# Kernel tuning notes

Hardware: AMD Instinct MI355X
Metric: run time of the kernel (lower is better)

Reference implementation:

```python
import jax, jax.numpy as jnp
import numpy as np

D_IN = 1024
D_OUT = 1024
NUM_HEADS = 16
HEAD_DIM = D_OUT // NUM_HEADS


def setup_inputs() -> dict:
    key = jax.random.key(0)
    ks = jax.random.split(key, 6)
    s = 0.02
    x = jax.random.normal(ks[0], (2, 2048, D_IN), dtype=jnp.float32)
    Wq = jax.random.normal(ks[1], (D_IN, D_OUT), dtype=jnp.float32) * s
    Wk = jax.random.normal(ks[2], (D_IN, D_OUT), dtype=jnp.float32) * s
    Wv = jax.random.normal(ks[3], (D_IN, D_OUT), dtype=jnp.float32) * s
    Wo = jax.random.normal(ks[4], (D_OUT, D_OUT), dtype=jnp.float32) * s
    bo = jnp.zeros((D_OUT,), dtype=jnp.float32)
    return {"x": x, "Wq": Wq, "Wk": Wk, "Wv": Wv, "Wo": Wo, "bo": bo}


def reference(x, Wq, Wk, Wv, Wo, bo):
    b, n, _ = x.shape
    # project and split heads: [b, h, n, d]
    def heads(W):
        return (x @ W).reshape(b, n, NUM_HEADS, HEAD_DIM).transpose(0, 2, 1, 3)
    q, k, v = heads(Wq), heads(Wk), heads(Wv)
    scores = jnp.einsum("bhqd,bhkd->bhqk", q, k)  # [b,h,n,n]
    causal = jnp.tril(jnp.ones((n, n), dtype=bool))  # True = keep
    scores = jnp.where(causal, scores, -jnp.inf)
    attn = jax.nn.softmax(scores / np.sqrt(HEAD_DIM).astype(np.float32), axis=-1)
    ctx = jnp.einsum("bhqk,bhkd->bhqd", attn, v)
    ctx = ctx.transpose(0, 2, 1, 3).reshape(b, n, D_OUT)
    return ctx @ Wo + bo
```

## Files before the change

### kernel.cpp

```cpp
#include <hip/hip_runtime.h>
#include <stdint.h>

typedef unsigned short u16;
typedef __attribute__((ext_vector_type(8))) __bf16 bf16x8;
typedef __attribute__((ext_vector_type(4))) float f32x4;
typedef __attribute__((ext_vector_type(16))) float f32x16;

#define D_IN 1024
#define NH 16
#define DH 64
#define BATCH 2
#define SEQ 2048

#define QSCL 0.1803368801111244f

#define GLD_LDS16(gp, lp)                                                              \
  __builtin_amdgcn_global_load_lds((__attribute__((address_space(1))) const void*)(gp), \
                                   (__attribute__((address_space(3))) void*)(lp), 16, 0, 0)

__device__ __forceinline__ u16 f2b(float f) {
  union { float ff; uint32_t u; } v; v.ff = f;
  return (u16)((v.u + 0x7fffu + ((v.u >> 16) & 1u)) >> 16);
}

__device__ __forceinline__ float swap32f(float v) { return __shfl_xor(v, 32, 64); }

__device__ __forceinline__ uint32_t cvtpk(float a, float b) {
  uint32_t r;
  asm("v_cvt_pk_bf16_f32 %0, %1, %2" : "=v"(r) : "v"(a), "v"(b));
  return r;
}
__device__ __forceinline__ float fexp2(float x) {
  float r;
  asm("v_exp_f32 %0, %1" : "=v"(r) : "v"(x));
  return r;
}

__global__ __launch_bounds__(256)
void prep_kernel(const float* __restrict__ x, u16* __restrict__ xb,
                 const float* __restrict__ W0, const float* __restrict__ W1,
                 const float* __restrict__ W2, const float* __restrict__ W3,
                 u16* __restrict__ T0, u16* __restrict__ T1,
                 u16* __restrict__ T2, u16* __restrict__ T3) {
  __shared__ float tile[32][33];
  if (blockIdx.x < 4096) {
    const int i = (blockIdx.x * 256 + threadIdx.x) * 4;
    const float4 v = *(const float4*)(x + i);
    uint2 pack;
    pack.x = (uint32_t)f2b(v.x) | ((uint32_t)f2b(v.y) << 16);
    pack.y = (uint32_t)f2b(v.z) | ((uint32_t)f2b(v.w) << 16);
    *(uint2*)(xb + i) = pack;
  } else {
    const int bid2 = blockIdx.x - 4096;
    const float* W; u16* T;
    switch (bid2 >> 10) {
      case 0: W = W0; T = T0; break;
      case 1: W = W1; T = T1; break;
      case 2: W = W2; T = T2; break;
      default: W = W3; T = T3; break;
    }
    const int rem = bid2 & 1023;
    const int n0 = (rem >> 5) * 32, k0 = (rem & 31) * 32;
    const int tx = threadIdx.x & 31, ty = threadIdx.x >> 5;
    #pragma unroll
    for (int i = 0; i < 32; i += 8)
      tile[ty + i][tx] = W[(size_t)(k0 + ty + i) * D_IN + n0 + tx];
    __syncthreads();
    #pragma unroll
    for (int i = 0; i < 32; i += 8)
      T[(size_t)(n0 + ty + i) * D_IN + k0 + tx] = f2b(tile[tx][ty + i]);
  }
}

__device__ __forceinline__ void qkv_compute(
    const u16* __restrict__ AsB, const u16* __restrict__ Bq,
    const u16* __restrict__ Bk, const u16* __restrict__ Bv,
    int wm, int wn, int g, int lm,
    f32x4 accq[4][2], f32x4 acck[4][2], f32x4 accv[4][2]) {
  #pragma unroll
  for (int kk = 0; kk < 2; ++kk) {
    const int slot = ((kk * 4 + g) ^ (lm & 7)) << 3;
    bf16x8 af[4];
    #pragma unroll
    for (int i = 0; i < 4; ++i)
      af[i] = *(const bf16x8*)(AsB + (wm * 64 + i * 16 + lm) * 64 + slot);
    bf16x8 bq[2], bk[2], bv[2];
    #pragma unroll
    for (int n = 0; n < 2; ++n) {
      const int ro = (wn * 32 + n * 16 + lm) * 64 + slot;
      bq[n] = *(const bf16x8*)(Bq + ro);
      bk[n] = *(const bf16x8*)(Bk + ro);
      bv[n] = *(const bf16x8*)(Bv + ro);
    }
    #pragma unroll
    for (int i = 0; i < 4; ++i)
      #pragma unroll
      for (int n = 0; n < 2; ++n) {
        accq[i][n] = __builtin_amdgcn_mfma_f32_16x16x32_bf16(af[i], bq[n], accq[i][n], 0, 0, 0);
        acck[i][n] = __builtin_amdgcn_mfma_f32_16x16x32_bf16(af[i], bk[n], acck[i][n], 0, 0, 0);
        accv[i][n] = __builtin_amdgcn_mfma_f32_16x16x32_bf16(af[i], bv[n], accv[i][n], 0, 0, 0);
      }
  }
}

__global__ __launch_bounds__(512)
void gemm_qkv_kernel(const u16* __restrict__ Xb,
                     const u16* __restrict__ WqT, const u16* __restrict__ WkT,
                     const u16* __restrict__ WvT,
                     u16* __restrict__ Qo, u16* __restrict__ Ko, u16* __restrict__ Vt) {
  __shared__ u16 As[2][128 * 64];
  __shared__ u16 Bs[2][3][128 * 64];

  const int tid = threadIdx.x;
  const int lane = tid & 63;
  const int w = tid >> 6;
  const int wm = w >> 2, wn = w & 3;
  const int bm = blockIdx.x * 128;
  const int bn = blockIdx.y * 128;
  const int g = lane >> 4, lm = lane & 15;

  const int r_in = lane >> 3;
  const int s_w = lane & 7;
  const int swz_col = (s_w ^ r_in) << 3;

  const int c0 = w * 2;
  const u16* a_src0 = Xb + (size_t)(bm + c0 * 8 + r_in) * D_IN + swz_col;
  const u16* a_src1 = a_src0 + 8 * D_IN;
  const u16* q_src0 = WqT + (size_t)(bn + c0 * 8 + r_in) * D_IN + swz_col;
  const u16* q_src1 = q_src0 + 8 * D_IN;
  const u16* k_src0 = WkT + (size_t)(bn + c0 * 8 + r_in) * D_IN + swz_col;
  const u16* k_src1 = k_src0 + 8 * D_IN;
  const u16* v_src0 = WvT + (size_t)(bn + c0 * 8 + r_in) * D_IN + swz_col;
  const u16* v_src1 = v_src0 + 8 * D_IN;

#define QKV_STAGE(BUF, K0)                                 \
  do {                                                     \
    GLD_LDS16(a_src0 + (K0), &As[BUF][c0 * 512]);          \
    GLD_LDS16(a_src1 + (K0), &As[BUF][c0 * 512 + 512]);    \
    GLD_LDS16(q_src0 + (K0), &Bs[BUF][0][c0 * 512]);       \
    GLD_LDS16(q_src1 + (K0), &Bs[BUF][0][c0 * 512 + 512]); \
    GLD_LDS16(k_src0 + (K0), &Bs[BUF][1][c0 * 512]);       \
    GLD_LDS16(k_src1 + (K0), &Bs[BUF][1][c0 * 512 + 512]); \
    GLD_LDS16(v_src0 + (K0), &Bs[BUF][2][c0 * 512]);       \
    GLD_LDS16(v_src1 + (K0), &Bs[BUF][2][c0 * 512 + 512]); \
  } while (0)

  f32x4 accq[4][2], acck[4][2], accv[4][2];
  #pragma unroll
  for (int i = 0; i < 4; ++i)
    #pragma unroll
    for (int n = 0; n < 2; ++n) {
      accq[i][n] = {0.f, 0.f, 0.f, 0.f};
      acck[i][n] = {0.f, 0.f, 0.f, 0.f};
      accv[i][n] = {0.f, 0.f, 0.f, 0.f};
    }

  QKV_STAGE(0, 0);
  QKV_STAGE(1, 64);
  #pragma unroll 1
  for (int tt = 0; tt < 7; ++tt) {
    asm volatile("s_waitcnt vmcnt(8)" ::: "memory");
    __builtin_amdgcn_s_barrier();
    qkv_compute(As[0], Bs[0][0], Bs[0][1], Bs[0][2], wm, wn, g, lm, accq, acck, accv);
    __builtin_amdgcn_s_barrier();
    QKV_STAGE(0, (2 * tt + 2) * 64);
    asm volatile("s_waitcnt vmcnt(8)" ::: "memory");
    __builtin_amdgcn_s_barrier();
    qkv_compute(As[1], Bs[1][0], Bs[1][1], Bs[1][2], wm, wn, g, lm, accq, acck, accv);
    __builtin_amdgcn_s_barrier();
    QKV_STAGE(1, (2 * tt + 3) * 64);
  }
  asm volatile("s_waitcnt vmcnt(8)" ::: "memory");
  __builtin_amdgcn_s_barrier();
  qkv_compute(As[0], Bs[0][0], Bs[0][1], Bs[0][2], wm, wn, g, lm, accq, acck, accv);
  asm volatile("s_waitcnt vmcnt(0)" ::: "memory");
  __builtin_amdgcn_s_barrier();
  qkv_compute(As[1], Bs[1][0], Bs[1][1], Bs[1][2], wm, wn, g, lm, accq, acck, accv);
#undef QKV_STAGE

  #pragma unroll
  for (int i = 0; i < 4; ++i) {
    #pragma unroll
    for (int n = 0; n < 2; ++n) {
      #pragma unroll
      for (int r = 0; r < 4; ++r) {
        const int m = bm + wm * 64 + i * 16 + g * 4 + r;
        const int c = bn + wn * 32 + n * 16 + lm;
        const int b = m >> 11, nn = m & (SEQ - 1);
        const int h = c >> 6, d = c & (DH - 1);
        const int bh = b * NH + h;
        const int t = nn >> 5;
        {
          const u16 val = f2b(accq[i][n][r] * QSCL);
          const int st = d >> 4;
          const int lane2 = ((d >> 3) & 1) * 32 + (nn & 31);
          const int j = d & 7;
          Qo[((size_t)(bh * 64 + t) * 4 + st) * 512 + lane2 * 8 + j] = val;
        }
        {
          const u16 val = f2b(acck[i][n][r]);
          const int st = d >> 4;
          const int lane2 = ((d >> 3) & 1) * 32 + (nn & 31);
          const int j = d & 7;
          Ko[((size_t)(bh * 64 + t) * 4 + st) * 512 + lane2 * 8 + j] = val;
        }
        {
          const u16 val = f2b(accv[i][n][r]);
          const int n5 = nn & 31;
          const int f = (n5 >> 4) * 2 + (d >> 5);
          const int lane2 = ((n5 >> 2) & 1) * 32 + (d & 31);
          const int j = ((n5 >> 3) & 1) * 4 + (n5 & 3);
          Vt[((size_t)(bh * 64 + t) * 4 + f) * 512 + lane2 * 8 + j] = val;
        }
      }
    }
  }
}

__global__ __launch_bounds__(256)
void attn4_kernel(const u16* __restrict__ Qb, const u16* __restrict__ Kb,
                  const u16* __restrict__ Vt, u16* __restrict__ Ctx) {
  __shared__ float mbuf[4][32][64];
  __shared__ float lbuf[4][32];

  const int tid = threadIdx.x;
  const int lane = tid & 63;
  const int kw = tid >> 6;
  const int ql = lane & 31;
  const int hi = lane >> 5;
  const int bid = blockIdx.x;
  const int c = bid & 7;
  const int r = bid >> 3;
  const int jj = r & 31;
  const int bh = c + 8 * (r >> 5);
  const int b = bh >> 4, h = bh & 15;

  const u16* Qf = Qb + (size_t)bh * 64 * 2048;
  const u16* Kf = Kb + (size_t)bh * 64 * 2048;
  const u16* Vf = Vt + (size_t)bh * 64 * 2048;
  const int lofs = lane * 8;

  #pragma unroll 1
  for (int pass = 0; pass < 2; ++pass) {
    const int qt = pass ? (63 - jj) : jj;
    const int qb0 = qt * 32;

    bf16x8 qf[4];
    {
      const u16* qp = Qf + (size_t)qt * 2048 + lofs;
      #pragma unroll
      for (int st = 0; st < 4; ++st) qf[st] = *(const bf16x8*)(qp + st * 512);
    }

    f32x16 ctx0 = {0,0,0,0,0,0,0,0,0,0,0,0,0,0,0,0};
    f32x16 ctx1 = {0,0,0,0,0,0,0,0,0,0,0,0,0,0,0,0};
    float lacc[4] = {0.f, 0.f, 0.f, 0.f};

    bf16x8 kf[4], vf[4];
    if (kw <= qt) {
      {
        const u16* kp = Kf + (size_t)kw * 2048 + lofs;
        const u16* vp = Vf + (size_t)kw * 2048 + lofs;
        #pragma unroll
        for (int st = 0; st < 4; ++st) kf[st] = *(const bf16x8*)(kp + st * 512);
        #pragma unroll
        for (int f = 0; f < 4; ++f) vf[f] = *(const bf16x8*)(vp + f * 512);
      }
      #pragma unroll 2
      for (int t = kw; t <= qt; t += 4) {
        f32x16 s = {0,0,0,0,0,0,0,0,0,0,0,0,0,0,0,0};
        __builtin_amdgcn_s_setprio(1);
        #pragma unroll
        for (int st = 0; st < 4; ++st)
          s = __builtin_amdgcn_mfma_f32_32x32x16_bf16(kf[st], qf[st], s, 0, 0, 0);
        __builtin_amdgcn_s_setprio(0);

        const int tn = (t + 4 <= qt) ? (t + 4) : qt;
        {
          const u16* kp = Kf + (size_t)tn * 2048 + lofs;
          #pragma unroll
          for (int st = 0; st < 4; ++st) kf[st] = *(const bf16x8*)(kp + st * 512);
        }

        float p[16];
        if (t == qt) {
          #pragma unroll
          for (int cr = 0; cr < 16; ++cr) {
            const int kl = ((cr & 3) + 8 * (cr >> 2)) + 4 * hi;
            p[cr] = (kl > ql) ? 0.f : fexp2(s[cr]);
          }
        } else {
          #pragma unroll
          for (int cr = 0; cr < 16; ++cr) p[cr] = fexp2(s[cr]);
        }
        #pragma unroll
        for (int cr = 0; cr < 16; ++cr) lacc[cr & 3] += p[cr];

        __builtin_amdgcn_s_setprio(1);
        #pragma unroll
        for (int ks = 0; ks < 2; ++ks) {
          uint4 pw;
          pw.x = cvtpk(p[ks * 8 + 0], p[ks * 8 + 1]);
          pw.y = cvtpk(p[ks * 8 + 2], p[ks * 8 + 3]);
          pw.z = cvtpk(p[ks * 8 + 4], p[ks * 8 + 5]);
          pw.w = cvtpk(p[ks * 8 + 6], p[ks * 8 + 7]);
          union { uint4 u; bf16x8 v; } pa; pa.u = pw;
          ctx0 = __builtin_amdgcn_mfma_f32_32x32x16_bf16(vf[ks * 2 + 0], pa.v, ctx0, 0, 0, 0);
          ctx1 = __builtin_amdgcn_mfma_f32_32x32x16_bf16(vf[ks * 2 + 1], pa.v, ctx1, 0, 0, 0);
        }
        __builtin_amdgcn_s_setprio(0);

        {
          const u16* vp = Vf + (size_t)tn * 2048 + lofs;
          #pragma unroll
          for (int f = 0; f < 4; ++f) vf[f] = *(const bf16x8*)(vp + f * 512);
        }
      }
    }

    const float lloc = (lacc[0] + lacc[1]) + (lacc[2] + lacc[3]);
    const float lwv = lloc + swap32f(lloc);

    #pragma unroll
    for (int grp = 0; grp < 4; ++grp) {
      const int ch = grp * 2 + hi;
      f32x4 t0 = {ctx0[grp * 4 + 0], ctx0[grp * 4 + 1], ctx0[grp * 4 + 2], ctx0[grp * 4 + 3]};
      f32x4 t1 = {ctx1[grp * 4 + 0], ctx1[grp * 4 + 1], ctx1[grp * 4 + 2], ctx1[grp * 4 + 3]};
      *(f32x4*)&mbuf[kw][ql][(ch ^ ql) * 4 & 63]       = t0;
      *(f32x4*)&mbuf[kw][ql][((ch + 8) ^ ql) * 4 & 63] = t1;
    }
    if (lane < 32) lbuf[kw][ql] = lwv;
    __syncthreads();

    {
      const int ch0 = kw * 4 + hi * 2;
      f32x4 a0 = {0.f, 0.f, 0.f, 0.f}, a1 = {0.f, 0.f, 0.f, 0.f};
      #pragma unroll
      for (int p2 = 0; p2 < 4; ++p2) {
        a0 += *(const f32x4*)&mbuf[p2][ql][(ch0 ^ ql) * 4 & 63];
        a1 += *(const f32x4*)&mbuf[p2][ql][((ch0 + 1) ^ ql) * 4 & 63];
      }
      const float lt = (lbuf[0][ql] + lbuf[1][ql]) + (lbuf[2][ql] + lbuf[3][ql]);
      const float inv = __builtin_amdgcn_rcpf(lt);
      uint4 pw;
      pw.x = cvtpk(a0[0] * inv, a0[1] * inv);
      pw.y = cvtpk(a0[2] * inv, a0[3] * inv);
      pw.z = cvtpk(a1[0] * inv, a1[1] * inv);
      pw.w = cvtpk(a1[2] * inv, a1[3] * inv);
      *(uint4*)(Ctx + (size_t)(b * SEQ + qb0 + ql) * 1024 + h * 64 + kw * 16 + hi * 8) = pw;
    }
    __syncthreads();
  }
}

__device__ __forceinline__ void out_compute(
    const u16* __restrict__ AsB, const u16* __restrict__ BsB,
    int wr, int wc, int g, int lm, f32x4 acc[4][4]) {
  #pragma unroll
  for (int kk = 0; kk < 2; ++kk) {
    const int slot = ((kk * 4 + g) ^ (lm & 7)) << 3;
    bf16x8 af[4], bf[4];
    #pragma unroll
    for (int i = 0; i < 4; ++i)
      af[i] = *(const bf16x8*)(AsB + (wr * 64 + i * 16 + lm) * 64 + slot);
    #pragma unroll
    for (int n = 0; n < 4; ++n)
      bf[n] = *(const bf16x8*)(BsB + (wc * 64 + n * 16 + lm) * 64 + slot);
    #pragma unroll
    for (int i = 0; i < 4; ++i)
      #pragma unroll
      for (int n = 0; n < 4; ++n)
        acc[i][n] = __builtin_amdgcn_mfma_f32_16x16x32_bf16(af[i], bf[n], acc[i][n], 0, 0, 0);
  }
}

__global__ __launch_bounds__(256)
void gemm_out_kernel(const u16* __restrict__ Ctx, const u16* __restrict__ WoT,
                     const float* __restrict__ bo, float* __restrict__ out) {
  __shared__ u16 As[2][128 * 64];
  __shared__ u16 Bs[2][128 * 64];
  const int tid = threadIdx.x;
  const int lane = tid & 63;
  const int w = tid >> 6;
  const int bm = blockIdx.x * 128;
  const int bn = blockIdx.y * 128;
  const int wr = w >> 1, wc = w & 1;
  const int g = lane >> 4, lm = lane & 15;

  const int r_in = lane >> 3;
  const int s_w = lane & 7;
  const int swz_col = (s_w ^ r_in) << 3;

  const int c0 = w * 4;
  const u16* a_src = Ctx + (size_t)(bm + c0 * 8 + r_in) * D_IN + swz_col;
  const u16* b_src = WoT + (size_t)(bn + c0 * 8 + r_in) * D_IN + swz_col;

#define OUT_STAGE(BUF, K0)                                              \
  do {                                                                  \
    _Pragma("unroll")                                                   \
    for (int j = 0; j < 4; ++j) {                                       \
      GLD_LDS16(a_src + j * 8 * D_IN + (K0), &As[BUF][(c0 + j) * 512]); \
      GLD_LDS16(b_src + j * 8 * D_IN + (K0), &Bs[BUF][(c0 + j) * 512]); \
    }                                                                   \
  } while (0)

  f32x4 acc[4][4];
  #pragma unroll
  for (int i = 0; i < 4; ++i)
    #pragma unroll
    for (int n = 0; n < 4; ++n) acc[i][n] = {0.f, 0.f, 0.f, 0.f};

  OUT_STAGE(0, 0);
  OUT_STAGE(1, 64);
  #pragma unroll 1
  for (int tt = 0; tt < 7; ++tt) {
    asm volatile("s_waitcnt vmcnt(8)" ::: "memory");
    __builtin_amdgcn_s_barrier();
    out_compute(As[0], Bs[0], wr, wc, g, lm, acc);
    __builtin_amdgcn_s_barrier();
    OUT_STAGE(0, (2 * tt + 2) * 64);
    asm volatile("s_waitcnt vmcnt(8)" ::: "memory");
    __builtin_amdgcn_s_barrier();
    out_compute(As[1], Bs[1], wr, wc, g, lm, acc);
    __builtin_amdgcn_s_barrier();
    OUT_STAGE(1, (2 * tt + 3) * 64);
  }
  asm volatile("s_waitcnt vmcnt(8)" ::: "memory");
  __builtin_amdgcn_s_barrier();
  out_compute(As[0], Bs[0], wr, wc, g, lm, acc);
  asm volatile("s_waitcnt vmcnt(0)" ::: "memory");
  __builtin_amdgcn_s_barrier();
  out_compute(As[1], Bs[1], wr, wc, g, lm, acc);
#undef OUT_STAGE

  #pragma unroll
  for (int i = 0; i < 4; ++i)
    #pragma unroll
    for (int n = 0; n < 4; ++n)
      #pragma unroll
      for (int r = 0; r < 4; ++r) {
        const int m = bm + wr * 64 + i * 16 + g * 4 + r;
        const int cidx = bn + wc * 64 + n * 16 + lm;
        out[(size_t)m * 1024 + cidx] = acc[i][n][r] + bo[cidx];
      }
}

extern "C" void kernel_launch(void* const* d_in, const int* in_sizes, int n_in,
                              void* d_out, int out_size, void* d_ws, size_t ws_size,
                              hipStream_t stream) {
  (void)in_sizes; (void)n_in; (void)out_size; (void)ws_size;
  const float* x  = (const float*)d_in[0];
  const float* Wq = (const float*)d_in[1];
  const float* Wk = (const float*)d_in[2];
  const float* Wv = (const float*)d_in[3];
  const float* Wo = (const float*)d_in[4];
  const float* bo = (const float*)d_in[5];
  float* out = (float*)d_out;

  char* ws = (char*)d_ws;
  u16* xb  = (u16*)(ws);
  u16* WqT = (u16*)(ws + (8u << 20));
  u16* WkT = (u16*)(ws + (10u << 20));
  u16* WvT = (u16*)(ws + (12u << 20));
  u16* WoT = (u16*)(ws + (14u << 20));
  u16* Qb  = (u16*)(ws + (16u << 20));
  u16* Kb  = (u16*)(ws + (24u << 20));
  u16* Vt  = (u16*)(ws + (32u << 20));
  u16* Ctx = xb;

  prep_kernel<<<dim3(8192), 256, 0, stream>>>(x, xb, Wq, Wk, Wv, Wo, WqT, WkT, WvT, WoT);
  gemm_qkv_kernel<<<dim3(32, 8), 512, 0, stream>>>(xb, WqT, WkT, WvT, Qb, Kb, Vt);
  attn4_kernel<<<dim3(1024), 256, 0, stream>>>(Qb, Kb, Vt, Ctx);
  gemm_out_kernel<<<dim3(32, 8), 256, 0, stream>>>(Ctx, WoT, bo, out);
}
```

Measured before the change: 93.13 us.

## Stage QKV epilogue through LDS for coalesced 16-byte stores; drop setprio in attention

The QKV GEMM epilogue used to write each bf16 output with a scattered 2-byte global store into the MFMA-fragment layouts of Q, K and V^T. It now packs each wave's outputs into a per-wave LDS pool that reuses the GEMM staging buffer, then writes full 512-element fragments with coalesced uint4 stores. This removes the scattered store traffic at the cost of an extra LDS pass and a block-wide sync. Separately, the s_setprio bumps around the MFMA sections in the attention kernel are removed.

```diff
diff --git a/kernel.cpp b/kernel.cpp
--- a/kernel.cpp
+++ b/kernel.cpp
@@ -108,8 +108,9 @@
                      const u16* __restrict__ WqT, const u16* __restrict__ WkT,
                      const u16* __restrict__ WvT,
                      u16* __restrict__ Qo, u16* __restrict__ Ko, u16* __restrict__ Vt) {
-  __shared__ u16 As[2][128 * 64];
-  __shared__ u16 Bs[2][3][128 * 64];
+  __shared__ u16 smem[65536];
+  u16* As0 = smem;
+  u16* Bs0 = smem + 16384;
 
   const int tid = threadIdx.x;
   const int lane = tid & 63;
@@ -133,16 +134,16 @@
   const u16* v_src0 = WvT + (size_t)(bn + c0 * 8 + r_in) * D_IN + swz_col;
   const u16* v_src1 = v_src0 + 8 * D_IN;
 
-#define QKV_STAGE(BUF, K0)                                 \
-  do {                                                     \
-    GLD_LDS16(a_src0 + (K0), &As[BUF][c0 * 512]);          \
-    GLD_LDS16(a_src1 + (K0), &As[BUF][c0 * 512 + 512]);    \
-    GLD_LDS16(q_src0 + (K0), &Bs[BUF][0][c0 * 512]);       \
-    GLD_LDS16(q_src1 + (K0), &Bs[BUF][0][c0 * 512 + 512]); \
-    GLD_LDS16(k_src0 + (K0), &Bs[BUF][1][c0 * 512]);       \
-    GLD_LDS16(k_src1 + (K0), &Bs[BUF][1][c0 * 512 + 512]); \
-    GLD_LDS16(v_src0 + (K0), &Bs[BUF][2][c0 * 512]);       \
-    GLD_LDS16(v_src1 + (K0), &Bs[BUF][2][c0 * 512 + 512]); \
+#define QKV_STAGE(BUF, K0)                                            \
+  do {                                                                \
+    GLD_LDS16(a_src0 + (K0), As0 + (BUF)*8192 + c0 * 512);            \
+    GLD_LDS16(a_src1 + (K0), As0 + (BUF)*8192 + c0 * 512 + 512);      \
+    GLD_LDS16(q_src0 + (K0), Bs0 + (BUF)*24576 + c0 * 512);           \
+    GLD_LDS16(q_src1 + (K0), Bs0 + (BUF)*24576 + c0 * 512 + 512);     \
+    GLD_LDS16(k_src0 + (K0), Bs0 + (BUF)*24576 + 8192 + c0 * 512);    \
+    GLD_LDS16(k_src1 + (K0), Bs0 + (BUF)*24576 + 8192 + c0 * 512 + 512); \
+    GLD_LDS16(v_src0 + (K0), Bs0 + (BUF)*24576 + 16384 + c0 * 512);   \
+    GLD_LDS16(v_src1 + (K0), Bs0 + (BUF)*24576 + 16384 + c0 * 512 + 512); \
   } while (0)
 
   f32x4 accq[4][2], acck[4][2], accv[4][2];
@@ -161,59 +162,64 @@
   for (int tt = 0; tt < 7; ++tt) {
     asm volatile("s_waitcnt vmcnt(8)" ::: "memory");
     __builtin_amdgcn_s_barrier();
-    qkv_compute(As[0], Bs[0][0], Bs[0][1], Bs[0][2], wm, wn, g, lm, accq, acck, accv);
+    qkv_compute(As0, Bs0, Bs0 + 8192, Bs0 + 16384, wm, wn, g, lm, accq, acck, accv);
     __builtin_amdgcn_s_barrier();
     QKV_STAGE(0, (2 * tt + 2) * 64);
     asm volatile("s_waitcnt vmcnt(8)" ::: "memory");
     __builtin_amdgcn_s_barrier();
-    qkv_compute(As[1], Bs[1][0], Bs[1][1], Bs[1][2], wm, wn, g, lm, accq, acck, accv);
+    qkv_compute(As0 + 8192, Bs0 + 24576, Bs0 + 32768, Bs0 + 40960, wm, wn, g, lm,
+                accq, acck, accv);
     __builtin_amdgcn_s_barrier();
     QKV_STAGE(1, (2 * tt + 3) * 64);
   }
   asm volatile("s_waitcnt vmcnt(8)" ::: "memory");
   __builtin_amdgcn_s_barrier();
-  qkv_compute(As[0], Bs[0][0], Bs[0][1], Bs[0][2], wm, wn, g, lm, accq, acck, accv);
+  qkv_compute(As0, Bs0, Bs0 + 8192, Bs0 + 16384, wm, wn, g, lm, accq, acck, accv);
   asm volatile("s_waitcnt vmcnt(0)" ::: "memory");
   __builtin_amdgcn_s_barrier();
-  qkv_compute(As[1], Bs[1][0], Bs[1][1], Bs[1][2], wm, wn, g, lm, accq, acck, accv);
+  qkv_compute(As0 + 8192, Bs0 + 24576, Bs0 + 32768, Bs0 + 40960, wm, wn, g, lm,
+              accq, acck, accv);
 #undef QKV_STAGE
 
+  __syncthreads();
+  u16* pool = smem + w * 6144;
+  const int M0 = bm + wm * 64;
+  const int T0v = (M0 & (SEQ - 1)) >> 5;
+  const int C0 = bn + wn * 32;
+  const int D0 = C0 & 63;
+  const int S0 = D0 >> 4;
+  const int d5 = D0 >> 5;
+  const int bh = (M0 >> 11) * NH + (C0 >> 6);
+
   #pragma unroll
   for (int i = 0; i < 4; ++i) {
+    const int ti = i >> 1;
+    const int nbase = (i & 1) * 16 + g * 4;
     #pragma unroll
     for (int n = 0; n < 2; ++n) {
       #pragma unroll
       for (int r = 0; r < 4; ++r) {
-        const int m = bm + wm * 64 + i * 16 + g * 4 + r;
-        const int c = bn + wn * 32 + n * 16 + lm;
-        const int b = m >> 11, nn = m & (SEQ - 1);
-        const int h = c >> 6, d = c & (DH - 1);
-        const int bh = b * NH + h;
-        const int t = nn >> 5;
-        {
-          const u16 val = f2b(accq[i][n][r] * QSCL);
-          const int st = d >> 4;
-          const int lane2 = ((d >> 3) & 1) * 32 + (nn & 31);
-          const int j = d & 7;
-          Qo[((size_t)(bh * 64 + t) * 4 + st) * 512 + lane2 * 8 + j] = val;
-        }
-        {
-          const u16 val = f2b(acck[i][n][r]);
-          const int st = d >> 4;
-          const int lane2 = ((d >> 3) & 1) * 32 + (nn & 31);
-          const int j = d & 7;
-          Ko[((size_t)(bh * 64 + t) * 4 + st) * 512 + lane2 * 8 + j] = val;
-        }
-        {
-          const u16 val = f2b(accv[i][n][r]);
-          const int n5 = nn & 31;
-          const int f = (n5 >> 4) * 2 + (d >> 5);
-          const int lane2 = ((n5 >> 2) & 1) * 32 + (d & 31);
-          const int j = ((n5 >> 3) & 1) * 4 + (n5 & 3);
-          Vt[((size_t)(bh * 64 + t) * 4 + f) * 512 + lane2 * 8 + j] = val;
-        }
-      }
-    }
+        const int offqk = (ti * 2 + n) * 512 + (((lm >> 3) << 5) + nbase + r) * 8 + (lm & 7);
+        pool[offqk] = f2b(accq[i][n][r] * QSCL);
+        pool[2048 + offqk] = f2b(acck[i][n][r]);
+        const int offv = 4096 + (ti * 2 + (i & 1)) * 512 +
+                         ((g & 1) * 32 + n * 16 + lm) * 8 + ((g >> 1) << 2) + r;
+        pool[offv] = f2b(accv[i][n][r]);
+      }
+    }
+  }
+  asm volatile("s_waitcnt lgkmcnt(0)" ::: "memory");
+  #pragma unroll
+  for (int fl = 0; fl < 4; ++fl) {
+    const int t = T0v + (fl >> 1);
+    const int st = S0 + (fl & 1);
+    const uint4 vq = *(const uint4*)(pool + fl * 512 + lane * 8);
+    *(uint4*)(Qo + ((size_t)(bh * 64 + t) * 4 + st) * 512 + lane * 8) = vq;
+    const uint4 vk = *(const uint4*)(pool + 2048 + fl * 512 + lane * 8);
+    *(uint4*)(Ko + ((size_t)(bh * 64 + t) * 4 + st) * 512 + lane * 8) = vk;
+    const int f = ((fl & 1) << 1) + d5;
+    const uint4 vv = *(const uint4*)(pool + 4096 + fl * 512 + lane * 8);
+    *(uint4*)(Vt + ((size_t)(bh * 64 + t) * 4 + f) * 512 + lane * 8) = vv;
   }
 }
 
@@ -269,11 +275,9 @@
       #pragma unroll 2
       for (int t = kw; t <= qt; t += 4) {
         f32x16 s = {0,0,0,0,0,0,0,0,0,0,0,0,0,0,0,0};
-        __builtin_amdgcn_s_setprio(1);
         #pragma unroll
         for (int st = 0; st < 4; ++st)
           s = __builtin_amdgcn_mfma_f32_32x32x16_bf16(kf[st], qf[st], s, 0, 0, 0);
-        __builtin_amdgcn_s_setprio(0);
 
         const int tn = (t + 4 <= qt) ? (t + 4) : qt;
         {
@@ -296,7 +300,6 @@
         #pragma unroll
         for (int cr = 0; cr < 16; ++cr) lacc[cr & 3] += p[cr];
 
-        __builtin_amdgcn_s_setprio(1);
         #pragma unroll
         for (int ks = 0; ks < 2; ++ks) {
           uint4 pw;
@@ -308,7 +311,6 @@
           ctx0 = __builtin_amdgcn_mfma_f32_32x32x16_bf16(vf[ks * 2 + 0], pa.v, ctx0, 0, 0, 0);
           ctx1 = __builtin_amdgcn_mfma_f32_32x32x16_bf16(vf[ks * 2 + 1], pa.v, ctx1, 0, 0, 0);
         }
-        __builtin_amdgcn_s_setprio(0);
 
         {
           const u16* vp = Vf + (size_t)tn * 2048 + lofs;
```

Result: faster. 88.29 us (-5.2%).
